# Kernel optimization log

Hardware: AMD Instinct MI355X
Metric: run time of the kernel (lower is better)

Reference implementation:

```python
import jax, jax.numpy as jnp
import numpy as np

N_EMBD = 1024
N_HEAD = 16
HEAD_DIM = N_EMBD // N_HEAD


def setup_inputs() -> dict:
    key = jax.random.key(0)
    k1, k2, k3 = jax.random.split(key, 3)
    x = jax.random.normal(k1, (2, 2048, N_EMBD), dtype=jnp.float32)
    # torch nn.Linear(in, out) weight has shape (out, in); y = x @ W.T
    w_qkv = jax.random.normal(k2, (3 * N_EMBD, N_EMBD), dtype=jnp.float32) * (1.0 / np.sqrt(N_EMBD))
    w_proj = jax.random.normal(k3, (N_EMBD, N_EMBD), dtype=jnp.float32) * (1.0 / np.sqrt(N_EMBD))
    return {"x": x, "w_qkv": w_qkv, "w_proj": w_proj}


def reference(x, w_qkv, w_proj):
    B, T, C = x.shape
    qkv = jnp.einsum('btc,dc->btd', x, w_qkv)  # [B,T,3C]
    q, k, v = jnp.split(qkv, 3, axis=2)
    # [B,H,T,hd]
    q = q.reshape(B, T, N_HEAD, HEAD_DIM).transpose(0, 2, 1, 3)
    k = k.reshape(B, T, N_HEAD, HEAD_DIM).transpose(0, 2, 1, 3)
    v = v.reshape(B, T, N_HEAD, HEAD_DIM).transpose(0, 2, 1, 3)
    att = jnp.einsum('bhqd,bhkd->bhqk', q, k) / jnp.sqrt(jnp.float32(HEAD_DIM))
    causal = jnp.tril(jnp.ones((T, T), dtype=bool))  # [T,T]
    att = jnp.where(causal[None, None], att, -jnp.inf)
    att = jax.nn.softmax(att, axis=-1)
    y = jnp.einsum('bhqk,bhkd->bhqd', att, v)
    y = y.transpose(0, 2, 1, 3).reshape(B, T, C)
    return jnp.einsum('btc,dc->btd', y, w_proj)
```

## Files before the change

### kernel.cpp

```cpp
#include <hip/hip_runtime.h>
#include <stdint.h>


typedef unsigned short u16;
typedef __bf16 bf16_t;
typedef bf16_t bf16x8 __attribute__((ext_vector_type(8)));
typedef float f32x4 __attribute__((ext_vector_type(4)));
typedef float f32x16 __attribute__((ext_vector_type(16)));

__device__ __forceinline__ u16 f2bf(float f) {
  return __builtin_bit_cast(u16, (bf16_t)f);
}

__device__ __forceinline__ float hexp2(float x) {
  float r;
  asm("v_exp_f32 %0, %1" : "=v"(r) : "v"(x));
  return r;
}
__device__ __forceinline__ uint32_t cvtpk(float lo, float hi) {
  uint32_t d;
  asm("v_cvt_pk_bf16_f32 %0, %1, %2" : "=v"(d) : "v"(lo), "v"(hi));
  return d;
}
__device__ __forceinline__ void plswap(uint32_t& a, uint32_t& b) {
  asm("v_permlane32_swap_b32 %0, %1" : "+v"(a), "+v"(b));
}

template<int CC>
__device__ __forceinline__ bf16x8 mkPfrag(const float* p) {
  uint32_t A1 = cvtpk(p[8 * CC + 0], p[8 * CC + 1]);
  uint32_t A2 = cvtpk(p[8 * CC + 2], p[8 * CC + 3]);
  uint32_t B1 = cvtpk(p[8 * CC + 4], p[8 * CC + 5]);
  uint32_t B2 = cvtpk(p[8 * CC + 6], p[8 * CC + 7]);
  plswap(A1, B1);
  plswap(A2, B2);
  union { uint32_t u[4]; bf16x8 v; } r;
  r.u[0] = A1; r.u[1] = A2; r.u[2] = B1; r.u[3] = B2;
  return r.v;
}

__device__ __forceinline__ void gload_lds16(const void* g, void* l) {
  __builtin_amdgcn_global_load_lds(
      (const __attribute__((address_space(1))) uint32_t*)(uint64_t)g,
      (__attribute__((address_space(3))) uint32_t*)(uint32_t)(uint64_t)l,
      16, 0, 0);
}

__global__ void cast_all(const float* __restrict__ x, const float* __restrict__ wq,
                         const float* __restrict__ wp, u16* __restrict__ xb,
                         u16* __restrict__ wqb, u16* __restrict__ wpb) {
  int i = blockIdx.x * blockDim.x + threadIdx.x;
  const float* s; u16* d; int off;
  if (i < 1048576)            { s = x;  d = xb;  off = i; }
  else if (i < 1048576 + 786432) { s = wq; d = wqb; off = i - 1048576; }
  else                        { s = wp; d = wpb; off = i - (1048576 + 786432); }
  float4 f = reinterpret_cast<const float4*>(s)[off];
  ushort4 o;
  o.x = f2bf(f.x); o.y = f2bf(f.y); o.z = f2bf(f.z); o.w = f2bf(f.w);
  reinterpret_cast<ushort4*>(d)[off] = o;
}

__global__ void gemm_qkv(const u16* __restrict__ A, const u16* __restrict__ Bm,
                         u16* __restrict__ qb, u16* __restrict__ kb,
                         u16* __restrict__ vb) {
  __shared__ __attribute__((aligned(16))) u16 SMEM[2 * 128 * 64];
  const int tid = threadIdx.x;
  const int lane = tid & 63;
  const int w = tid >> 6;
  const int wr = w >> 1, wc = w & 1;
  const int g = lane >> 4, r = lane & 15;
  const int bid = blockIdx.x + 24 * blockIdx.y;
  const int xcd = bid & 7, idx = bid >> 3;
  const int tn = (xcd & 1) * 12 + (idx % 12);
  const int tm = (xcd >> 1) * 8 + (idx / 12);

  f32x4 acc[4][4] = {};

  const char* Ab = (const char*)(A + (size_t)tm * 128 * 1024);
  const char* Bb = (const char*)(Bm + (size_t)tn * 128 * 1024);
  char* AsB = (char*)SMEM;
  char* BsB = AsB + 16384;

  for (int k0 = 0; k0 < 1024; k0 += 64) {
#pragma unroll
    for (int i = 0; i < 4; ++i) {
      const int L = (i * 256 + tid) * 16;
      const int row = L >> 7;
      const int colb = (L & 127) ^ ((row & 7) << 4);
      gload_lds16(Ab + (size_t)row * 2048 + k0 * 2 + colb, AsB + L);
      gload_lds16(Bb + (size_t)row * 2048 + k0 * 2 + colb, BsB + L);
    }
    __syncthreads();
#pragma unroll
    for (int kk = 0; kk < 2; ++kk) {
      bf16x8 a[4], b[4];
#pragma unroll
      for (int m = 0; m < 4; ++m) {
        const int rowA = wr * 64 + m * 16 + r;
        const int kbyt = (kk * 64 + g * 16) ^ ((rowA & 7) << 4);
        a[m] = *(const bf16x8*)(AsB + rowA * 128 + kbyt);
      }
#pragma unroll
      for (int n = 0; n < 4; ++n) {
        const int rowB = wc * 64 + n * 16 + r;
        const int kbyt = (kk * 64 + g * 16) ^ ((rowB & 7) << 4);
        b[n] = *(const bf16x8*)(BsB + rowB * 128 + kbyt);
      }
      __builtin_amdgcn_s_setprio(1);
#pragma unroll
      for (int m = 0; m < 4; ++m)
#pragma unroll
        for (int n = 0; n < 4; ++n)
          acc[m][n] = __builtin_amdgcn_mfma_f32_16x16x32_bf16(a[m], b[n], acc[m][n], 0, 0, 0);
      __builtin_amdgcn_s_setprio(0);
    }
    __syncthreads();
  }

  const int mrow0 = tm * 128 + wr * 64;
  const int ncol0 = tn * 128 + wc * 64;
  const int sel = (tn * 128) >> 10;
  const float qscl = (sel == 0) ? 0.18033688f : 1.0f;
  if (sel < 2) {
    u16* dst = (sel == 0) ? qb : kb;
#pragma unroll
    for (int m = 0; m < 4; ++m)
#pragma unroll
      for (int n = 0; n < 4; ++n) {
        const int nc = (ncol0 + n * 16 + r) & 1023;
        const int h = nc >> 6, d = nc & 63;
#pragma unroll
        for (int j = 0; j < 4; ++j) {
          const int mr = mrow0 + m * 16 + g * 4 + j;
          const int bb = mr >> 11, t = mr & 2047;
          dst[((size_t)(bb * 16 + h) * 2048 + t) * 64 + d] = f2bf(acc[m][n][j] * qscl);
        }
      }
  } else {
    u16* Wv = SMEM + w * 4096;
#pragma unroll
    for (int m = 0; m < 4; ++m)
#pragma unroll
      for (int n = 0; n < 4; ++n) {
        const int dl = n * 16 + r;
        uint32_t lo = cvtpk(acc[m][n][0], acc[m][n][1]);
        uint32_t hi2 = cvtpk(acc[m][n][2], acc[m][n][3]);
        char* p = (char*)Wv + dl * 128 + ((m * 32 + g * 8) ^ ((dl & 7) << 4));
        *(uint32_t*)p = lo;
        *(uint32_t*)(p + 4) = hi2;
      }
    asm volatile("s_waitcnt lgkmcnt(0)" ::: "memory");
    __builtin_amdgcn_sched_barrier(0);
    const int hh = (ncol0 - 2048) >> 6;
    const int t0 = mrow0 & 2047;
    const int bb2 = mrow0 >> 11;
    u16* vdst = vb + ((size_t)(bb2 * 16 + hh) * 64) * 2048 + t0;
#pragma unroll
    for (int rd = 0; rd < 8; ++rd) {
      const int dl = rd * 8 + (lane >> 3);
      const int tb = lane & 7;
      const char* src = (char*)Wv + dl * 128 + ((tb ^ (dl & 7)) << 4);
      *(uint4*)(vdst + (size_t)dl * 2048 + tb * 8) = *(const uint4*)src;
    }
  }
}

__global__ void gemm_out(const u16* __restrict__ A, const u16* __restrict__ Bm,
                         float* __restrict__ outf) {
  __shared__ __attribute__((aligned(16))) u16 SMEM[24576];
  const int tid = threadIdx.x;
  const int lane = tid & 63;
  const int w = tid >> 6;
  const int g = lane >> 4, r = lane & 15;
  const int bid = blockIdx.x + 8 * blockIdx.y;
  const int xcd = bid & 7, idx = bid >> 3;
  const int tn = (xcd & 3) * 2 + (idx & 1);
  const int tm = ((xcd >> 2) << 5) + (idx >> 1);

  f32x4 acc[4][2] = {};

  const char* Ab = (const char*)(A + (size_t)tm * 64 * 1024);
  const char* Bb = (const char*)(Bm + (size_t)tn * 128 * 1024);

  auto stage = [&](int t, int buf) {
    char* AsD = (char*)SMEM + buf * 24576;
    char* BsD = AsD + 8192;
#pragma unroll
    for (int i = 0; i < 2; ++i) {
      const int L = (i * 256 + tid) * 16;
      const int row = L >> 7;
      const int colb = (L & 127) ^ ((row & 7) << 4);
      gload_lds16(Ab + (size_t)row * 2048 + t * 128 + colb, AsD + L);
    }
#pragma unroll
    for (int i = 0; i < 4; ++i) {
      const int L = (i * 256 + tid) * 16;
      const int row = L >> 7;
      const int colb = (L & 127) ^ ((row & 7) << 4);
      gload_lds16(Bb + (size_t)row * 2048 + t * 128 + colb, BsD + L);
    }
  };

  stage(0, 0);
  for (int t = 0; t < 16; ++t) {
    if (t < 15) {
      stage(t + 1, (t + 1) & 1);
      asm volatile("s_waitcnt vmcnt(6)" ::: "memory");
    } else {
      asm volatile("s_waitcnt vmcnt(0)" ::: "memory");
    }
    __builtin_amdgcn_s_barrier();
    __builtin_amdgcn_sched_barrier(0);
    const char* AsB = (const char*)SMEM + (t & 1) * 24576;
    const char* BsB = AsB + 8192;
#pragma unroll
    for (int kk = 0; kk < 2; ++kk) {
      bf16x8 a[4], b[2];
#pragma unroll
      for (int m = 0; m < 4; ++m) {
        const int rowA = m * 16 + r;
        const int kbyt = (kk * 64 + g * 16) ^ ((rowA & 7) << 4);
        a[m] = *(const bf16x8*)(AsB + rowA * 128 + kbyt);
      }
#pragma unroll
      for (int n = 0; n < 2; ++n) {
        const int rowB = w * 32 + n * 16 + r;
        const int kbyt = (kk * 64 + g * 16) ^ ((rowB & 7) << 4);
        b[n] = *(const bf16x8*)(BsB + rowB * 128 + kbyt);
      }
      __builtin_amdgcn_s_setprio(1);
#pragma unroll
      for (int m = 0; m < 4; ++m)
#pragma unroll
        for (int n = 0; n < 2; ++n)
          acc[m][n] = __builtin_amdgcn_mfma_f32_16x16x32_bf16(a[m], b[n], acc[m][n], 0, 0, 0);
      __builtin_amdgcn_s_setprio(0);
    }
    __builtin_amdgcn_sched_barrier(0);
    __builtin_amdgcn_s_barrier();
  }

  const int mrow0 = tm * 64;
  const int ncol0 = tn * 128 + w * 32;
#pragma unroll
  for (int m = 0; m < 4; ++m)
#pragma unroll
    for (int n = 0; n < 2; ++n) {
      const int nc = ncol0 + n * 16 + r;
#pragma unroll
      for (int j = 0; j < 4; ++j) {
        const int mr = mrow0 + m * 16 + g * 4 + j;
        outf[(size_t)mr * 1024 + nc] = acc[m][n][j];
      }
    }
}

__global__ __launch_bounds__(256, 2)
void attn_fwd(const u16* __restrict__ qb, const u16* __restrict__ kb,
              const u16* __restrict__ vb, u16* __restrict__ yb) {
  __shared__ __attribute__((aligned(16))) u16 Ks[2][128 * 64];
  __shared__ __attribute__((aligned(16))) u16 Vs[2][64 * 128];
  __shared__ __attribute__((aligned(16))) float Linv[4][32];
  const int tid = threadIdx.x;
  const int lane = tid & 63;
  const int w = tid >> 6;
  const int hi = lane >> 5;
  const int q5 = lane & 31;
  const int hi4 = hi * 4;
  const int bh = blockIdx.x;
  const int bb = bh >> 4, h = bh & 15;
  const int base = (blockIdx.y + bh) & 15;
  const int a = (base < 8) ? 2 * base : 31 - 2 * base;
  const int qb0 = a * 128;
  const int qw = qb0 + w * 32;
  const int qg = qw + q5;

  const char* Kb = (const char*)(kb + (size_t)bh * (2048 * 64));
  const char* Vb = (const char*)(vb + (size_t)bh * (64 * 2048));
  const u16* Q = qb + (size_t)bh * (2048 * 64);

  bf16x8 qf[4];
#pragma unroll
  for (int f = 0; f < 4; ++f)
    qf[f] = *(const bf16x8*)(&Q[(size_t)qg * 64 + f * 16 + hi * 8]);

  f32x16 o0 = {}, o1 = {};
  float ps0 = 0.f, ps1 = 0.f, ps2 = 0.f, ps3 = 0.f;

  const int nph = a + 1;
  const int swzK = (q5 & 7) << 4;
  const int swzV = (q5 & 15) << 4;

  auto stage = [&](int p, int buf) {
#pragma unroll
    for (int i = 0; i < 4; ++i) {
      const int L = (i * 256 + tid) * 16;
      const int row = L >> 7;
      const int colb = (L & 127) ^ ((row & 7) << 4);
      gload_lds16(Kb + ((size_t)p * 128 + row) * 128 + colb, (char*)Ks[buf] + L);
    }
#pragma unroll
    for (int i = 0; i < 4; ++i) {
      const int L = (i * 256 + tid) * 16;
      const int row = L >> 8;
      const int colb = (L & 255) ^ ((row & 15) << 4);
      gload_lds16(Vb + (size_t)row * 4096 + (size_t)p * 256 + colb, (char*)Vs[buf] + L);
    }
  };

  auto compute = [&](int p, const char* KsB, const char* VsB) {
#pragma unroll
    for (int hh = 0; hh < 4; ++hh) {
      const int kh = p * 128 + hh * 32;
      if (kh <= qw + 31) {
        f32x16 s = {};
        __builtin_amdgcn_s_setprio(1);
#pragma unroll
        for (int f = 0; f < 4; ++f) {
          bf16x8 ka = *(const bf16x8*)(KsB + (hh * 32 + q5) * 128 + ((f * 32 + hi * 16) ^ swzK));
          s = __builtin_amdgcn_mfma_f32_32x32x16_bf16(ka, qf[f], s, 0, 0, 0);
        }
        __builtin_amdgcn_s_setprio(0);

        float pv[16];
        if (kh + 31 > qw) {
#pragma unroll
          for (int i = 0; i < 16; ++i) {
            const int kl = (i & 3) + 8 * (i >> 2) + hi4;
            float e = hexp2(s[i]);
            pv[i] = (kh + kl <= qg) ? e : 0.0f;
          }
        } else {
#pragma unroll
          for (int i = 0; i < 16; ++i)
            pv[i] = hexp2(s[i]);
        }
#pragma unroll
        for (int i = 0; i < 16; i += 4) {
          ps0 += pv[i];
          ps1 += pv[i + 1];
          ps2 += pv[i + 2];
          ps3 += pv[i + 3];
        }

        bf16x8 pf0 = mkPfrag<0>(pv);
        bf16x8 pf1 = mkPfrag<1>(pv);

        __builtin_amdgcn_s_setprio(1);
#pragma unroll
        for (int c = 0; c < 2; ++c) {
          const int cc = hh * 2 + c;
          const int cb = cc * 32 + hi * 16;
          bf16x8 v0f = *(const bf16x8*)(VsB + q5 * 256 + (cb ^ swzV));
          bf16x8 v1f = *(const bf16x8*)(VsB + (32 + q5) * 256 + (cb ^ swzV));
          const bf16x8 pf = c ? pf1 : pf0;
          o0 = __builtin_amdgcn_mfma_f32_32x32x16_bf16(pf, v0f, o0, 0, 0, 0);
          o1 = __builtin_amdgcn_mfma_f32_32x32x16_bf16(pf, v1f, o1, 0, 0, 0);
        }
        __builtin_amdgcn_s_setprio(0);
      }
    }
  };

  stage(0, 0);
  for (int t = 0; t < nph; ++t) {
    const int pn = (t + 1 < nph) ? t + 1 : 0;
    stage(pn, (t + 1) & 1);
    asm volatile("s_waitcnt vmcnt(8)" ::: "memory");
    __builtin_amdgcn_s_barrier();
    __builtin_amdgcn_sched_barrier(0);
    compute(t, (const char*)Ks[t & 1], (const char*)Vs[t & 1]);
    __builtin_amdgcn_sched_barrier(0);
    __builtin_amdgcn_s_barrier();
  }

  float psum = (ps0 + ps1) + (ps2 + ps3);
  const float tot = psum + __shfl_xor(psum, 32);
  if (lane < 32) Linv[w][q5] = 1.0f / tot;
  asm volatile("s_waitcnt lgkmcnt(0)" ::: "memory");
  __builtin_amdgcn_sched_barrier(0);
  f32x4 lv[4];
#pragma unroll
  for (int r2 = 0; r2 < 4; ++r2)
    lv[r2] = *(const f32x4*)(&Linv[w][r2 * 8 + hi4]);

#pragma unroll
  for (int reg = 0; reg < 16; ++reg) {
    const int r4 = reg & 3, r2 = reg >> 2;
    const float li = lv[r2][r4];
    const int trow = qw + r4 + 8 * r2 + hi4;
    const size_t bpos = ((size_t)(bb * 2048 + trow)) * 1024 + h * 64 + q5;
    yb[bpos]      = f2bf(o0[reg] * li);
    yb[bpos + 32] = f2bf(o1[reg] * li);
  }
}

extern "C" void kernel_launch(void* const* d_in, const int* in_sizes, int n_in,
                              void* d_out, int out_size, void* d_ws, size_t ws_size,
                              hipStream_t stream) {
  const float* x     = (const float*)d_in[0];
  const float* wqkv  = (const float*)d_in[1];
  const float* wproj = (const float*)d_in[2];
  float* out = (float*)d_out;
  char* ws = (char*)d_ws;
  u16* xb     = (u16*)(ws + (size_t)(0u  << 20));
  u16* wqkvb  = (u16*)(ws + (size_t)(8u  << 20));
  u16* wprojb = (u16*)(ws + (size_t)(14u << 20));
  u16* qb     = (u16*)(ws + (size_t)(16u << 20));
  u16* kb     = (u16*)(ws + (size_t)(24u << 20));
  u16* vb     = (u16*)(ws + (size_t)(32u << 20));
  u16* yb     = (u16*)(ws + (size_t)(40u << 20));

  cast_all<<<8192, 256, 0, stream>>>(x, wqkv, wproj, xb, wqkvb, wprojb);

  gemm_qkv<<<dim3(24, 32), 256, 0, stream>>>(xb, wqkvb, qb, kb, vb);
  attn_fwd<<<dim3(32, 16), 256, 0, stream>>>(qb, kb, vb, yb);
  gemm_out<<<dim3(8, 64), 256, 0, stream>>>(yb, wprojb, out);
}
```

Measured before the change: 86.89 us.

## Double-buffer QKV GEMM LDS loads and stage Q/K epilogue through LDS

```diff
diff --git a/kernel.cpp b/kernel.cpp
--- a/kernel.cpp
+++ b/kernel.cpp
@@ -63,7 +63,7 @@
 __global__ void gemm_qkv(const u16* __restrict__ A, const u16* __restrict__ Bm,
                          u16* __restrict__ qb, u16* __restrict__ kb,
                          u16* __restrict__ vb) {
-  __shared__ __attribute__((aligned(16))) u16 SMEM[2 * 128 * 64];
+  __shared__ __attribute__((aligned(16))) u16 SMEM[32768];
   const int tid = threadIdx.x;
   const int lane = tid & 63;
   const int w = tid >> 6;
@@ -78,19 +78,33 @@
 
   const char* Ab = (const char*)(A + (size_t)tm * 128 * 1024);
   const char* Bb = (const char*)(Bm + (size_t)tn * 128 * 1024);
-  char* AsB = (char*)SMEM;
-  char* BsB = AsB + 16384;
-
-  for (int k0 = 0; k0 < 1024; k0 += 64) {
+
+  auto stage = [&](int t, int buf) {
+    char* AsD = (char*)SMEM + buf * 32768;
+    char* BsD = AsD + 16384;
+    const int k0b = t * 128;
 #pragma unroll
     for (int i = 0; i < 4; ++i) {
       const int L = (i * 256 + tid) * 16;
       const int row = L >> 7;
       const int colb = (L & 127) ^ ((row & 7) << 4);
-      gload_lds16(Ab + (size_t)row * 2048 + k0 * 2 + colb, AsB + L);
-      gload_lds16(Bb + (size_t)row * 2048 + k0 * 2 + colb, BsB + L);
-    }
-    __syncthreads();
+      gload_lds16(Ab + (size_t)row * 2048 + k0b + colb, AsD + L);
+      gload_lds16(Bb + (size_t)row * 2048 + k0b + colb, BsD + L);
+    }
+  };
+
+  stage(0, 0);
+  for (int t = 0; t < 16; ++t) {
+    if (t < 15) {
+      stage(t + 1, (t + 1) & 1);
+      asm volatile("s_waitcnt vmcnt(8)" ::: "memory");
+    } else {
+      asm volatile("s_waitcnt vmcnt(0)" ::: "memory");
+    }
+    __builtin_amdgcn_s_barrier();
+    __builtin_amdgcn_sched_barrier(0);
+    const char* AsB = (const char*)SMEM + (t & 1) * 32768;
+    const char* BsB = AsB + 16384;
 #pragma unroll
     for (int kk = 0; kk < 2; ++kk) {
       bf16x8 a[4], b[4];
@@ -114,30 +128,42 @@
           acc[m][n] = __builtin_amdgcn_mfma_f32_16x16x32_bf16(a[m], b[n], acc[m][n], 0, 0, 0);
       __builtin_amdgcn_s_setprio(0);
     }
-    __syncthreads();
+    __builtin_amdgcn_sched_barrier(0);
+    __builtin_amdgcn_s_barrier();
   }
 
   const int mrow0 = tm * 128 + wr * 64;
   const int ncol0 = tn * 128 + wc * 64;
   const int sel = (tn * 128) >> 10;
-  const float qscl = (sel == 0) ? 0.18033688f : 1.0f;
+  u16* Wb = SMEM + w * 4096;
+
   if (sel < 2) {
+    const float qscl = (sel == 0) ? 0.18033688f : 1.0f;
+#pragma unroll
+    for (int m = 0; m < 4; ++m)
+#pragma unroll
+      for (int n = 0; n < 4; ++n)
+#pragma unroll
+        for (int j = 0; j < 4; ++j) {
+          const int tl = m * 16 + g * 4 + j;
+          const int d = n * 16 + r;
+          *(u16*)((char*)Wb + tl * 128 + ((d * 2) ^ ((tl & 7) << 4))) =
+              f2bf(acc[m][n][j] * qscl);
+        }
+    asm volatile("s_waitcnt lgkmcnt(0)" ::: "memory");
+    __builtin_amdgcn_sched_barrier(0);
     u16* dst = (sel == 0) ? qb : kb;
-#pragma unroll
-    for (int m = 0; m < 4; ++m)
-#pragma unroll
-      for (int n = 0; n < 4; ++n) {
-        const int nc = (ncol0 + n * 16 + r) & 1023;
-        const int h = nc >> 6, d = nc & 63;
-#pragma unroll
-        for (int j = 0; j < 4; ++j) {
-          const int mr = mrow0 + m * 16 + g * 4 + j;
-          const int bb = mr >> 11, t = mr & 2047;
-          dst[((size_t)(bb * 16 + h) * 2048 + t) * 64 + d] = f2bf(acc[m][n][j] * qscl);
-        }
-      }
+    const int h = (ncol0 & 1023) >> 6;
+    const int bb = mrow0 >> 11, t0 = mrow0 & 2047;
+    u16* drow = dst + ((size_t)(bb * 16 + h) * 2048 + t0) * 64;
+#pragma unroll
+    for (int it = 0; it < 8; ++it) {
+      const int tl = it * 8 + (lane >> 3);
+      const int cb = (lane & 7) * 16;
+      const char* src = (char*)Wb + tl * 128 + (cb ^ ((tl & 7) << 4));
+      *(uint4*)((char*)(drow + (size_t)tl * 64) + cb) = *(const uint4*)src;
+    }
   } else {
-    u16* Wv = SMEM + w * 4096;
 #pragma unroll
     for (int m = 0; m < 4; ++m)
 #pragma unroll
@@ -145,9 +171,8 @@
         const int dl = n * 16 + r;
         uint32_t lo = cvtpk(acc[m][n][0], acc[m][n][1]);
         uint32_t hi2 = cvtpk(acc[m][n][2], acc[m][n][3]);
-        char* p = (char*)Wv + dl * 128 + ((m * 32 + g * 8) ^ ((dl & 7) << 4));
-        *(uint32_t*)p = lo;
-        *(uint32_t*)(p + 4) = hi2;
+        char* p = (char*)Wb + dl * 128 + ((m * 32 + g * 8) ^ ((dl & 7) << 4));
+        *(uint64_t*)p = ((uint64_t)hi2 << 32) | lo;
       }
     asm volatile("s_waitcnt lgkmcnt(0)" ::: "memory");
     __builtin_amdgcn_sched_barrier(0);
@@ -159,7 +184,7 @@
     for (int rd = 0; rd < 8; ++rd) {
       const int dl = rd * 8 + (lane >> 3);
       const int tb = lane & 7;
-      const char* src = (char*)Wv + dl * 128 + ((tb ^ (dl & 7)) << 4);
+      const char* src = (char*)Wb + dl * 128 + ((tb ^ (dl & 7)) << 4);
       *(uint4*)(vdst + (size_t)dl * 2048 + tb * 8) = *(const uint4*)src;
     }
   }
```

After: 89.08 us. 1.03x slower.
